# Performance work log

Hardware: AMD Instinct MI355X
Metric: run time of the kernel (lower is better)

Reference implementation:

```python
import jax, jax.numpy as jnp
import numpy as np

N = 50000      # num nodes
E = 800000     # num edges
F_IN = 100     # input features (ogbn-products)
HID = 128      # hidden_dim (per-head out_channels)
H = 2          # heads
OUT = 47       # num classes
NEG_SLOPE = 0.2


def setup_inputs() -> dict:
    key = jax.random.key(0)
    ks = jax.random.split(key, 14)
    def glorot(k, shape, fan):
        return jax.random.normal(k, shape, jnp.float32) * (1.0 / np.sqrt(fan))
    x = jax.random.normal(ks[0], (N, F_IN), jnp.float32)
    edge_index = jax.random.randint(ks[1], (2, E), 0, N)
    # GAT layer 0: lin_l (= lin_r, shared) weight [H*HID, F_IN], attention vecs [H, HID]
    W0 = glorot(ks[2], (H * HID, F_IN), F_IN)
    b0 = jnp.zeros((H * HID,), jnp.float32)
    attl0 = glorot(ks[3], (H, HID), HID)
    attr0 = glorot(ks[4], (H, HID), HID)
    # GAT layer 1: input dim H*HID
    W1 = glorot(ks[5], (H * HID, H * HID), H * HID)
    b1 = jnp.zeros((H * HID,), jnp.float32)
    attl1 = glorot(ks[6], (H, HID), HID)
    attr1 = glorot(ks[7], (H, HID), HID)
    # post_mp: Linear(H*HID -> HID), Linear(HID -> OUT)
    Wp1 = glorot(ks[8], (HID, H * HID), H * HID)
    bp1 = jnp.zeros((HID,), jnp.float32)
    Wp2 = glorot(ks[9], (OUT, HID), HID)
    bp2 = jnp.zeros((OUT,), jnp.float32)
    return dict(x=x, edge_index=edge_index, W0=W0, b0=b0, attl0=attl0, attr0=attr0,
                W1=W1, b1=b1, attl1=attl1, attr1=attr1,
                Wp1=Wp1, bp1=bp1, Wp2=Wp2, bp2=bp2)


def gat_layer(x, W, b, att_l, att_r, src, dst):
    # shared lin_l == lin_r in the source
    h = (x @ W.T + b).reshape(-1, H, HID)          # [N, H, C]
    alpha_l = jnp.einsum('nhc,hc->nh', h, att_l)   # per-node left scores
    alpha_r = jnp.einsum('nhc,hc->nh', h, att_r)   # per-node right scores
    e = jax.nn.leaky_relu(alpha_l[src] + alpha_r[dst], NEG_SLOPE)  # [E, H]
    # segment softmax over edges grouped by destination node
    emax = jax.ops.segment_max(e, dst, num_segments=N)             # [N, H]
    ee = jnp.exp(e - emax[dst])
    denom = jax.ops.segment_sum(ee, dst, num_segments=N)           # [N, H]
    a = ee / denom[dst]                                            # [E, H]
    msg = a[:, :, None] * h[src]                                   # [E, H, C]
    out = jax.ops.segment_sum(msg, dst, num_segments=N)            # [N, H, C]
    return out.reshape(-1, H * HID)


def reference(x, edge_index, W0, b0, attl0, attr0, W1, b1, attl1, attr1, Wp1, bp1, Wp2, bp2):
    src, dst = edge_index[0], edge_index[1]
    x = jax.nn.relu(gat_layer(x, W0, b0, attl0, attr0, src, dst))
    x = jax.nn.relu(gat_layer(x, W1, b1, attl1, attr1, src, dst))
    h = x @ Wp1.T + bp1           # dropout p=0.0 -> identity
    logits = h @ Wp2.T + bp2
    return jax.nn.log_softmax(logits, axis=1)
```

## Files before the change

kernel.cpp:

```cpp
#include <hip/hip_runtime.h>
#include <math.h>

#define N_NODES 50000
#define E_EDGES 800000
#define F_IN 100
#define HID 128
#define HEADS 2
#define OUT_C 47
#define HH (HEADS*HID)
#define MPAD 50048

typedef float floatx4 __attribute__((ext_vector_type(4)));
typedef float float2v __attribute__((ext_vector_type(2)));
typedef short short8 __attribute__((ext_vector_type(8)));

__device__ inline ushort bf16round(float v) {
    unsigned u = __float_as_uint(v);
    return (ushort)((u + 0x7FFFu + ((u >> 16) & 1u)) >> 16);
}

__device__ __forceinline__ void gl_lds16(const void* g, void* l) {
    __builtin_amdgcn_global_load_lds(
        (const __attribute__((address_space(1))) unsigned int*)g,
        (__attribute__((address_space(3))) unsigned int*)l, 16, 0, 0);
}

__device__ __forceinline__ void gemm_body(
    int bx, int by,
    const ushort* __restrict__ Ab, const ushort* __restrict__ Wb,
    const float* __restrict__ bias,
    ushort* __restrict__ Hb,
    const float* __restrict__ attl, const float* __restrict__ attr,
    float* __restrict__ al, float* __restrict__ ar,
    int M, int Kp, ushort* sA, ushort* sB)
{
    const int t = threadIdx.x;
    const int wave = t >> 6, lane = t & 63;
    const int quad = lane >> 4, l16 = lane & 15;
    const int rl = lane >> 2, seg = lane & 3;
    const int m0 = by * 128, n0 = bx * 128;

    floatx4 acc[2][8];
#pragma unroll
    for (int i = 0; i < 2; i++)
#pragma unroll
        for (int j = 0; j < 8; j++) acc[i][j] = (floatx4)(0.f);

    for (int k0 = 0; k0 < Kp; k0 += 32) {
#pragma unroll
        for (int j = 0; j < 2; j++) {
            int br = wave * 32 + j * 16;
            size_t gro = (size_t)(m0 + br + rl) * Kp + k0 + seg * 8;
            gl_lds16(Ab + gro, sA + br * 32);
        }
#pragma unroll
        for (int j = 0; j < 2; j++) {
            int br = wave * 32 + j * 16;
            size_t gro = (size_t)(n0 + br + rl) * Kp + k0 + seg * 8;
            gl_lds16(Wb + gro, sB + br * 32);
        }
        __syncthreads();

        short8 af[2];
#pragma unroll
        for (int sm = 0; sm < 2; sm++) {
            int r = wave * 32 + sm * 16 + l16;
            af[sm] = *(const short8*)(sA + r * 32 + quad * 8);
        }
#pragma unroll
        for (int sn = 0; sn < 8; sn++) {
            int r = sn * 16 + l16;
            short8 b = *(const short8*)(sB + r * 32 + quad * 8);
#pragma unroll
            for (int sm = 0; sm < 2; sm++)
                acc[sm][sn] = __builtin_amdgcn_mfma_f32_16x16x32_bf16(af[sm], b, acc[sm][sn], 0, 0, 0);
        }
        __syncthreads();
    }

    float bias_r[8], att_l[8], att_r[8];
#pragma unroll
    for (int sn = 0; sn < 8; sn++) {
        int ai = n0 + sn * 16 + l16;
        bias_r[sn] = bias[ai];
        att_l[sn] = attl[ai];
        att_r[sn] = attr[ai];
    }
#pragma unroll
    for (int sm = 0; sm < 2; sm++)
#pragma unroll
        for (int r = 0; r < 4; r++) {
            int gm = m0 + wave * 32 + sm * 16 + quad * 4 + r;
            float suml = 0.f, sumr = 0.f;
#pragma unroll
            for (int sn = 0; sn < 8; sn++) {
                float v = acc[sm][sn][r] + bias_r[sn];
                suml += v * att_l[sn];
                sumr += v * att_r[sn];
                if (gm < M) {
                    int gn = n0 + sn * 16 + l16;
                    Hb[(size_t)gm * 256 + gn] = bf16round(v);
                }
            }
#pragma unroll
            for (int off = 1; off < 16; off <<= 1) {
                suml += __shfl_xor(suml, off);
                sumr += __shfl_xor(sumr, off);
            }
            if (l16 == 0 && gm < M) {
                al[gm * HEADS + bx] = suml;
                ar[gm * HEADS + bx] = sumr;
            }
        }
}

__global__ __launch_bounds__(256) void gemm_l0(
    const ushort* __restrict__ xb, const ushort* __restrict__ W0b,
    const float* __restrict__ b0,
    const float* __restrict__ attl0, const float* __restrict__ attr0,
    ushort* __restrict__ hb, float* __restrict__ al, float* __restrict__ ar)
{
    __shared__ ushort sA[128 * 32], sB[128 * 32];
    gemm_body(blockIdx.x, blockIdx.y, xb, W0b, b0,
              hb, attl0, attr0, al, ar, N_NODES, 128, sA, sB);
}

__global__ __launch_bounds__(256) void gemm_l1(
    const ushort* __restrict__ Ab, const ushort* __restrict__ Wb,
    const float* __restrict__ bias, ushort* __restrict__ Hb,
    const float* __restrict__ attl, const float* __restrict__ attr,
    float* __restrict__ al, float* __restrict__ ar)
{
    __shared__ ushort sA[128 * 32], sB[128 * 32];
    gemm_body(blockIdx.x, blockIdx.y, Ab, Wb, bias,
              Hb, attl, attr, al, ar, N_NODES, HH, sA, sB);
}

__global__ void count_convert(const int* __restrict__ dstv, int* __restrict__ deg,
                              ushort* __restrict__ rank,
                              const float* __restrict__ x,  const float* __restrict__ W0,
                              const float* __restrict__ W1, const float* __restrict__ Wp1,
                              const float* __restrict__ Wp2,
                              ushort* __restrict__ xb,  ushort* __restrict__ W0b,
                              ushort* __restrict__ W1b, ushort* __restrict__ Wp1b,
                              ushort* __restrict__ Wp2b) {
    const int cx = N_NODES * 32;
    const int c0 = cx + 256 * 32;
    const int c1 = c0 + (HH * HH) / 4;
    const int c2 = c1 + (HID * HH) / 4;
    const int c3 = c2 + (64 * HID) / 4;
    int i = blockIdx.x * 256 + threadIdx.x;
    if (i < E_EDGES) {
        int d = dstv[i];
        rank[i] = (ushort)atomicAdd(&deg[d], 1);
    }
    if (i >= c3) return;
    float4 v = make_float4(0.f, 0.f, 0.f, 0.f);
    ushort* H; size_t o;
    if (i < cx) {
        int row = i >> 5, kc = (i & 31) * 4;
        if (kc < F_IN) v = *(const float4*)(x + (size_t)row * F_IN + kc);
        H = xb; o = (size_t)row * 128 + kc;
    } else if (i < c0) {
        int j = i - cx;
        int row = j >> 5, kc = (j & 31) * 4;
        if (kc < F_IN) v = *(const float4*)(W0 + (size_t)row * F_IN + kc);
        H = W0b; o = (size_t)row * 128 + kc;
    } else if (i < c1) {
        int j = i - c0;
        v = *(const float4*)(W1 + (size_t)j * 4);
        H = W1b; o = (size_t)j * 4;
    } else if (i < c2) {
        int j = i - c1;
        v = *(const float4*)(Wp1 + (size_t)j * 4);
        H = Wp1b; o = (size_t)j * 4;
    } else {
        int j = i - c2;
        int row = j >> 5;
        if (row < OUT_C) v = *(const float4*)(Wp2 + (size_t)j * 4);
        H = Wp2b; o = (size_t)j * 4;
    }
    ushort4 r;
    r.x = bf16round(v.x); r.y = bf16round(v.y);
    r.z = bf16round(v.z); r.w = bf16round(v.w);
    *(ushort4*)(H + o) = r;
}

__global__ void scan_local(const int* __restrict__ cnt, int* __restrict__ excl,
                           int* __restrict__ bsum, int Nn) {
    __shared__ int s[256];
    int t = threadIdx.x;
    int i = blockIdx.x * 256 + t;
    int v = (i < Nn) ? cnt[i] : 0;
    s[t] = v;
    __syncthreads();
    for (int off = 1; off < 256; off <<= 1) {
        int add = (t >= off) ? s[t - off] : 0;
        __syncthreads();
        s[t] += add;
        __syncthreads();
    }
    int incl = s[t];
    if (i < Nn) excl[i] = incl - v;
    if (t == 255) bsum[blockIdx.x] = incl;
}

__global__ void scan_add_fused(int* __restrict__ rowptr, const int* __restrict__ bsum,
                               int Nn, int Etot, int nblk) {
    __shared__ int s[256];
    int t = threadIdx.x;
    s[t] = (t < nblk) ? bsum[t] : 0;
    __syncthreads();
    for (int off = 1; off < 256; off <<= 1) {
        int add = (t >= off) ? s[t - off] : 0;
        __syncthreads();
        s[t] += add;
        __syncthreads();
    }
    int add = (blockIdx.x == 0) ? 0 : s[blockIdx.x - 1];
    int i = blockIdx.x * 256 + t;
    if (i < Nn) rowptr[i] += add;
    if (i == 0) rowptr[Nn] = Etot;
}

__global__ void fill_csr16(const int* __restrict__ src, const int* __restrict__ dst,
                           const int* __restrict__ rowptr, const ushort* __restrict__ rank,
                           ushort* __restrict__ csr16, int E) {
    int e = blockIdx.x * 256 + threadIdx.x;
    if (e < E) {
        int pos = rowptr[dst[e]] + (int)rank[e];
        csr16[pos] = (ushort)src[e];
    }
}

__global__ __launch_bounds__(256) void gat_aggregate(
    const ushort* __restrict__ hb, const float* __restrict__ al, const float* __restrict__ ar,
    const int* __restrict__ rowptr, const ushort* __restrict__ csr16,
    ushort* __restrict__ outb)
{
    const int node = blockIdx.x * 4 + (threadIdx.x >> 6);
    const int lane = threadIdx.x & 63;
    if (node >= N_NODES) return;
    const int beg = rowptr[node], end = rowptr[node + 1];
    const int half = lane >> 5;
    const int l32  = lane & 31;
    const int headf = l32 >> 4;
    const float2 ard = ((const float2*)ar)[node];

    float dsum0 = 0.f, dsum1 = 0.f;
    float2v av[4];
#pragma unroll
    for (int j = 0; j < 4; j++) av[j] = (float2v)(0.f);

    for (int c0 = beg; c0 < end; c0 += 64) {
        const int n = min(64, end - c0);
        int s = 0; float w0 = 0.f, w1 = 0.f;
        if (lane < n) {
            s = (int)csr16[c0 + lane];
            float2 aa = ((const float2*)al)[s];
            float e0 = aa.x + ard.x;
            float e1 = aa.y + ard.y;
            e0 = fmaxf(e0, 0.f) + 0.2f * fminf(e0, 0.f);
            e1 = fmaxf(e1, 0.f) + 0.2f * fminf(e1, 0.f);
            w0 = __expf(e0); w1 = __expf(e1);
            dsum0 += w0; dsum1 += w1;
        }
        for (int i = 0; i < n; i += 4) {
            int e0i = i + half;
            int   se0 = __shfl(s,  e0i);
            float u00 = __shfl(w0, e0i);
            float u01 = __shfl(w1, e0i);
            float2v we0 = (float2v)(headf ? u01 : u00);
            const uint4 q0 = *(const uint4*)(hb + (size_t)se0 * 256 + l32 * 8);
            int e1i = i + 2 + half;
            int   se1 = __shfl(s,  e1i);
            float u10 = __shfl(w0, e1i);
            float u11 = __shfl(w1, e1i);
            float2v we1 = (float2v)(headf ? u11 : u10);
            const uint4 q1 = *(const uint4*)(hb + (size_t)se1 * 256 + l32 * 8);
            float2v p;
            p.x = __uint_as_float(q0.x << 16); p.y = __uint_as_float(q0.x & 0xFFFF0000u);
            av[0] += we0 * p;
            p.x = __uint_as_float(q0.y << 16); p.y = __uint_as_float(q0.y & 0xFFFF0000u);
            av[1] += we0 * p;
            p.x = __uint_as_float(q0.z << 16); p.y = __uint_as_float(q0.z & 0xFFFF0000u);
            av[2] += we0 * p;
            p.x = __uint_as_float(q0.w << 16); p.y = __uint_as_float(q0.w & 0xFFFF0000u);
            av[3] += we0 * p;
            p.x = __uint_as_float(q1.x << 16); p.y = __uint_as_float(q1.x & 0xFFFF0000u);
            av[0] += we1 * p;
            p.x = __uint_as_float(q1.y << 16); p.y = __uint_as_float(q1.y & 0xFFFF0000u);
            av[1] += we1 * p;
            p.x = __uint_as_float(q1.z << 16); p.y = __uint_as_float(q1.z & 0xFFFF0000u);
            av[2] += we1 * p;
            p.x = __uint_as_float(q1.w << 16); p.y = __uint_as_float(q1.w & 0xFFFF0000u);
            av[3] += we1 * p;
        }
    }
#pragma unroll
    for (int j = 0; j < 4; j++) {
        av[j].x += __shfl_xor(av[j].x, 32);
        av[j].y += __shfl_xor(av[j].y, 32);
    }
#pragma unroll
    for (int off = 32; off; off >>= 1) {
        dsum0 += __shfl_xor(dsum0, off);
        dsum1 += __shfl_xor(dsum1, off);
    }
    if (half == 0) {
        const float den = headf ? dsum1 : dsum0;
        const float inv = (end > beg) ? 1.f / den : 0.f;
        ushort r[8];
#pragma unroll
        for (int j = 0; j < 4; j++) {
            r[2*j]   = bf16round(fmaxf(av[j].x * inv, 0.f));
            r[2*j+1] = bf16round(fmaxf(av[j].y * inv, 0.f));
        }
        *(uint4*)(outb + (size_t)node * 256 + l32 * 8) = *(uint4*)r;
    }
}

__global__ __launch_bounds__(256) void fused_post(
    const ushort* __restrict__ Ab,
    const ushort* __restrict__ Bb,
    const float* __restrict__ bp1,
    const ushort* __restrict__ W2b,
    const float* __restrict__ bp2,
    float* __restrict__ out, int M)
{
    __shared__ ushort sA[128 * 32];
    __shared__ ushort sB[128 * 32];
    __shared__ ushort sP[128 * 136];

    const int t = threadIdx.x;
    const int wave = t >> 6, lane = t & 63;
    const int quad = lane >> 4, l16 = lane & 15;
    const int rl = lane >> 2, seg = lane & 3;
    const int m0 = blockIdx.x * 128;

    floatx4 acc[2][8];
#pragma unroll
    for (int i = 0; i < 2; i++)
#pragma unroll
        for (int j = 0; j < 8; j++) acc[i][j] = (floatx4)(0.f);

    for (int k0 = 0; k0 < HH; k0 += 32) {
#pragma unroll
        for (int j = 0; j < 2; j++) {
            int br = wave * 32 + j * 16;
            size_t gro = (size_t)(m0 + br + rl) * HH + k0 + seg * 8;
            gl_lds16(Ab + gro, sA + br * 32);
        }
#pragma unroll
        for (int j = 0; j < 2; j++) {
            int br = wave * 32 + j * 16;
            size_t gro = (size_t)(br + rl) * HH + k0 + seg * 8;
            gl_lds16(Bb + gro, sB + br * 32);
        }
        __syncthreads();
        short8 af[2];
#pragma unroll
        for (int sm = 0; sm < 2; sm++) {
            int r = wave * 32 + sm * 16 + l16;
            af[sm] = *(const short8*)(sA + r * 32 + quad * 8);
        }
#pragma unroll
        for (int sn = 0; sn < 8; sn++) {
            int r = sn * 16 + l16;
            short8 b = *(const short8*)(sB + r * 32 + quad * 8);
#pragma unroll
            for (int sm = 0; sm < 2; sm++)
                acc[sm][sn] = __builtin_amdgcn_mfma_f32_16x16x32_bf16(af[sm], b, acc[sm][sn], 0, 0, 0);
        }
        __syncthreads();
    }
#pragma unroll
    for (int sm = 0; sm < 2; sm++)
#pragma unroll
        for (int sn = 0; sn < 8; sn++)
#pragma unroll
            for (int r = 0; r < 4; r++) {
                int row = wave * 32 + sm * 16 + quad * 4 + r;
                int col = sn * 16 + l16;
                sP[row * 136 + col] = bf16round(acc[sm][sn][r] + bp1[col]);
            }
    __syncthreads();

    floatx4 acc2[2][4];
#pragma unroll
    for (int i = 0; i < 2; i++)
#pragma unroll
        for (int j = 0; j < 4; j++) acc2[i][j] = (floatx4)(0.f);

    for (int k0 = 0; k0 < HID; k0 += 32) {
        {
            int br = wave * 16;
            size_t gro = (size_t)(br + rl) * HID + k0 + seg * 8;
            gl_lds16(W2b + gro, sA + br * 32);
        }
        __syncthreads();
        short8 ph[2];
#pragma unroll
        for (int sm = 0; sm < 2; sm++) {
            int r = wave * 32 + sm * 16 + l16;
            ph[sm] = *(const short8*)(sP + r * 136 + k0 + quad * 8);
        }
#pragma unroll
        for (int sn = 0; sn < 4; sn++) {
            int r = sn * 16 + l16;
            short8 b = *(const short8*)(sA + r * 32 + quad * 8);
#pragma unroll
            for (int sm = 0; sm < 2; sm++)
                acc2[sm][sn] = __builtin_amdgcn_mfma_f32_16x16x32_bf16(ph[sm], b, acc2[sm][sn], 0, 0, 0);
        }
        __syncthreads();
    }

    float b2[4];
#pragma unroll
    for (int sn = 0; sn < 4; sn++) {
        int n = sn * 16 + l16;
        b2[sn] = (n < OUT_C) ? bp2[n] : 0.f;
    }
#pragma unroll
    for (int sm = 0; sm < 2; sm++)
#pragma unroll
        for (int r = 0; r < 4; r++) {
            float v[4];
            float m = -INFINITY;
#pragma unroll
            for (int sn = 0; sn < 4; sn++) {
                int n = sn * 16 + l16;
                float xv = (n < OUT_C) ? acc2[sm][sn][r] + b2[sn] : -INFINITY;
                v[sn] = xv;
                m = fmaxf(m, xv);
            }
#pragma unroll
            for (int off = 1; off < 16; off <<= 1) m = fmaxf(m, __shfl_xor(m, off));
            float ssum = 0.f;
#pragma unroll
            for (int sn = 0; sn < 4; sn++) {
                int n = sn * 16 + l16;
                if (n < OUT_C) ssum += __expf(v[sn] - m);
            }
#pragma unroll
            for (int off = 1; off < 16; off <<= 1) ssum += __shfl_xor(ssum, off);
            float lse = m + logf(ssum);
            int gm = m0 + wave * 32 + sm * 16 + quad * 4 + r;
            if (gm < M) {
#pragma unroll
                for (int sn = 0; sn < 4; sn++) {
                    int n = sn * 16 + l16;
                    if (n < OUT_C) out[(size_t)gm * OUT_C + n] = v[sn] - lse;
                }
            }
        }
}

extern "C" void kernel_launch(void* const* d_in, const int* in_sizes, int n_in,
                              void* d_out, int out_size, void* d_ws, size_t ws_size,
                              hipStream_t stream) {
    const float* x     = (const float*)d_in[0];
    const int*   ei    = (const int*)d_in[1];
    const float* W0    = (const float*)d_in[2];
    const float* b0    = (const float*)d_in[3];
    const float* attl0 = (const float*)d_in[4];
    const float* attr0 = (const float*)d_in[5];
    const float* W1    = (const float*)d_in[6];
    const float* b1    = (const float*)d_in[7];
    const float* attl1 = (const float*)d_in[8];
    const float* attr1 = (const float*)d_in[9];
    const float* Wp1   = (const float*)d_in[10];
    const float* bp1   = (const float*)d_in[11];
    const float* Wp2   = (const float*)d_in[12];
    const float* bp2   = (const float*)d_in[13];
    float* out = (float*)d_out;

    const int Nn = N_NODES, Etot = E_EDGES;
    const int* srcv = ei;
    const int* dstv = ei + Etot;

    char* ws = (char*)d_ws;
    size_t off = 0;
    auto alloc = [&](size_t bytes) -> void* {
        void* p = ws + off;
        off = (off + bytes + 255) & ~(size_t)255;
        return p;
    };
    int*    rowptr = (int*)alloc((size_t)(Nn + 1) * sizeof(int));
    int*    deg    = (int*)alloc((size_t)Nn * sizeof(int));
    ushort* rank   = (ushort*)alloc((size_t)Etot * 2);
    ushort* csr16  = (ushort*)alloc((size_t)Etot * 2);
    int*    bsum   = (int*)alloc(256 * sizeof(int));
    float*  al     = (float*)alloc((size_t)Nn * HEADS * sizeof(float));
    float*  ar     = (float*)alloc((size_t)Nn * HEADS * sizeof(float));
    ushort* xb     = (ushort*)alloc((size_t)MPAD * 128 * 2);
    ushort* W0b    = (ushort*)alloc((size_t)HH * 128 * 2);
    ushort* W1b    = (ushort*)alloc((size_t)HH * HH * 2);
    ushort* Wp1b   = (ushort*)alloc((size_t)HID * HH * 2);
    ushort* Wp2b   = (ushort*)alloc((size_t)64 * HID * 2);
    ushort* hb     = (ushort*)alloc((size_t)Nn * HH * 2);
    ushort* xbb    = (ushort*)alloc((size_t)MPAD * HH * 2);

    const int nblk = (Nn + 255) / 256;

    hipMemsetAsync(deg, 0, (size_t)Nn * sizeof(int), stream);

    {
        const int tot = N_NODES * 32 + 256 * 32 + (HH * HH) / 4 + (HID * HH) / 4 + (64 * HID) / 4;
        const int grid = (tot + 255) / 256;
        count_convert<<<grid, 256, 0, stream>>>(
            dstv, deg, rank, x, W0, W1, Wp1, Wp2, xb, W0b, W1b, Wp1b, Wp2b);
    }

    {
        dim3 g(2, MPAD / 128);
        gemm_l0<<<g, 256, 0, stream>>>(xb, W0b, b0, attl0, attr0, hb, al, ar);
    }

    scan_local<<<nblk, 256, 0, stream>>>(deg, rowptr, bsum, Nn);
    scan_add_fused<<<nblk, 256, 0, stream>>>(rowptr, bsum, Nn, Etot, nblk);
    fill_csr16<<<(Etot + 255) / 256, 256, 0, stream>>>(srcv, dstv, rowptr, rank, csr16, Etot);

    gat_aggregate<<<(Nn + 3) / 4, 256, 0, stream>>>(hb, al, ar, rowptr, csr16, xbb);

    {
        dim3 g(2, MPAD / 128);
        gemm_l1<<<g, 256, 0, stream>>>(xbb, W1b, b1, hb, attl1, attr1, al, ar);
    }
    gat_aggregate<<<(Nn + 3) / 4, 256, 0, stream>>>(hb, al, ar, rowptr, csr16, xbb);

    fused_post<<<MPAD / 128, 256, 0, stream>>>(xbb, Wp1b, bp1, Wp2b, bp2, out, Nn);
}
```

Before: 313.7 us.

## Fuse CSR build and bf16 conversion into one cooperative kernel with grid syncs

Replaces the memset, count_convert, two scan kernels and fill_csr16 with a single cooperative kernel of 196 blocks that uses grid.sync between phases. This removes several kernel launches and their inter-kernel gaps. In exchange, a small persistent grid does all the edge atomics and the conversion through grid-stride loops, which lowers parallelism. It also depends on all 196 blocks being co-resident.

```diff
diff --git a/kernel.cpp b/kernel.cpp
--- a/kernel.cpp
+++ b/kernel.cpp
@@ -1,5 +1,8 @@
 #include <hip/hip_runtime.h>
+#include <hip/hip_cooperative_groups.h>
 #include <math.h>
+
+namespace cg = cooperative_groups;
 
 #define N_NODES 50000
 #define E_EDGES 800000
@@ -9,6 +12,7 @@
 #define OUT_C 47
 #define HH (HEADS*HID)
 #define MPAD 50048
+#define NBLK 196
 
 typedef float floatx4 __attribute__((ext_vector_type(4)));
 typedef float float2v __attribute__((ext_vector_type(2)));
@@ -23,6 +27,101 @@
     __builtin_amdgcn_global_load_lds(
         (const __attribute__((address_space(1))) unsigned int*)g,
         (__attribute__((address_space(3))) unsigned int*)l, 16, 0, 0);
+}
+
+__global__ void csr_build(
+    const int* __restrict__ dstv, const int* __restrict__ srcv,
+    int* __restrict__ deg, ushort* __restrict__ rank,
+    int* __restrict__ rowptr, int* __restrict__ bsum, ushort* __restrict__ csr16,
+    const float* __restrict__ x,  const float* __restrict__ W0,
+    const float* __restrict__ W1, const float* __restrict__ Wp1,
+    const float* __restrict__ Wp2,
+    ushort* __restrict__ xb,  ushort* __restrict__ W0b,
+    ushort* __restrict__ W1b, ushort* __restrict__ Wp1b, ushort* __restrict__ Wp2b)
+{
+    cg::grid_group grid = cg::this_grid();
+    const int t = threadIdx.x;
+    const int tid = blockIdx.x * 256 + t;
+    const int gsz = NBLK * 256;
+
+    for (int i = tid; i < N_NODES; i += gsz) deg[i] = 0;
+    grid.sync();
+
+    for (int e = tid; e < E_EDGES; e += gsz)
+        rank[e] = (ushort)atomicAdd(&deg[dstv[e]], 1);
+    {
+        const int cx = N_NODES * 32;
+        const int c0 = cx + 256 * 32;
+        const int c1 = c0 + (HH * HH) / 4;
+        const int c2 = c1 + (HID * HH) / 4;
+        const int c3 = c2 + (64 * HID) / 4;
+        for (int i = tid; i < c3; i += gsz) {
+            float4 v = make_float4(0.f, 0.f, 0.f, 0.f);
+            ushort* H; size_t o;
+            if (i < cx) {
+                int row = i >> 5, kc = (i & 31) * 4;
+                if (kc < F_IN) v = *(const float4*)(x + (size_t)row * F_IN + kc);
+                H = xb; o = (size_t)row * 128 + kc;
+            } else if (i < c0) {
+                int j = i - cx;
+                int row = j >> 5, kc = (j & 31) * 4;
+                if (kc < F_IN) v = *(const float4*)(W0 + (size_t)row * F_IN + kc);
+                H = W0b; o = (size_t)row * 128 + kc;
+            } else if (i < c1) {
+                int j = i - c0;
+                v = *(const float4*)(W1 + (size_t)j * 4);
+                H = W1b; o = (size_t)j * 4;
+            } else if (i < c2) {
+                int j = i - c1;
+                v = *(const float4*)(Wp1 + (size_t)j * 4);
+                H = Wp1b; o = (size_t)j * 4;
+            } else {
+                int j = i - c2;
+                int row = j >> 5;
+                if (row < OUT_C) v = *(const float4*)(Wp2 + (size_t)j * 4);
+                H = Wp2b; o = (size_t)j * 4;
+            }
+            ushort4 r;
+            r.x = bf16round(v.x); r.y = bf16round(v.y);
+            r.z = bf16round(v.z); r.w = bf16round(v.w);
+            *(ushort4*)(H + o) = r;
+        }
+    }
+    grid.sync();
+
+    __shared__ int s[256];
+    int i2 = blockIdx.x * 256 + t;
+    int v2 = (i2 < N_NODES) ? deg[i2] : 0;
+    s[t] = v2;
+    __syncthreads();
+    for (int off = 1; off < 256; off <<= 1) {
+        int add = (t >= off) ? s[t - off] : 0;
+        __syncthreads();
+        s[t] += add;
+        __syncthreads();
+    }
+    int incl = s[t];
+    if (i2 < N_NODES) rowptr[i2] = incl - v2;
+    if (t == 255) bsum[blockIdx.x] = incl;
+    grid.sync();
+
+    s[t] = (t < NBLK) ? bsum[t] : 0;
+    __syncthreads();
+    for (int off = 1; off < 256; off <<= 1) {
+        int add = (t >= off) ? s[t - off] : 0;
+        __syncthreads();
+        s[t] += add;
+        __syncthreads();
+    }
+    int addp = (blockIdx.x == 0) ? 0 : s[blockIdx.x - 1];
+    if (i2 < N_NODES) rowptr[i2] += addp;
+    if (i2 == 0) rowptr[N_NODES] = E_EDGES;
+    grid.sync();
+
+    for (int e = tid; e < E_EDGES; e += gsz) {
+        int pos = rowptr[dstv[e]] + (int)rank[e];
+        csr16[pos] = (ushort)srcv[e];
+    }
 }
 
 __device__ __forceinline__ void gemm_body(
@@ -134,103 +233,6 @@
     __shared__ ushort sA[128 * 32], sB[128 * 32];
     gemm_body(blockIdx.x, blockIdx.y, Ab, Wb, bias,
               Hb, attl, attr, al, ar, N_NODES, HH, sA, sB);
-}
-
-__global__ void count_convert(const int* __restrict__ dstv, int* __restrict__ deg,
-                              ushort* __restrict__ rank,
-                              const float* __restrict__ x,  const float* __restrict__ W0,
-                              const float* __restrict__ W1, const float* __restrict__ Wp1,
-                              const float* __restrict__ Wp2,
-                              ushort* __restrict__ xb,  ushort* __restrict__ W0b,
-                              ushort* __restrict__ W1b, ushort* __restrict__ Wp1b,
-                              ushort* __restrict__ Wp2b) {
-    const int cx = N_NODES * 32;
-    const int c0 = cx + 256 * 32;
-    const int c1 = c0 + (HH * HH) / 4;
-    const int c2 = c1 + (HID * HH) / 4;
-    const int c3 = c2 + (64 * HID) / 4;
-    int i = blockIdx.x * 256 + threadIdx.x;
-    if (i < E_EDGES) {
-        int d = dstv[i];
-        rank[i] = (ushort)atomicAdd(&deg[d], 1);
-    }
-    if (i >= c3) return;
-    float4 v = make_float4(0.f, 0.f, 0.f, 0.f);
-    ushort* H; size_t o;
-    if (i < cx) {
-        int row = i >> 5, kc = (i & 31) * 4;
-        if (kc < F_IN) v = *(const float4*)(x + (size_t)row * F_IN + kc);
-        H = xb; o = (size_t)row * 128 + kc;
-    } else if (i < c0) {
-        int j = i - cx;
-        int row = j >> 5, kc = (j & 31) * 4;
-        if (kc < F_IN) v = *(const float4*)(W0 + (size_t)row * F_IN + kc);
-        H = W0b; o = (size_t)row * 128 + kc;
-    } else if (i < c1) {
-        int j = i - c0;
-        v = *(const float4*)(W1 + (size_t)j * 4);
-        H = W1b; o = (size_t)j * 4;
-    } else if (i < c2) {
-        int j = i - c1;
-        v = *(const float4*)(Wp1 + (size_t)j * 4);
-        H = Wp1b; o = (size_t)j * 4;
-    } else {
-        int j = i - c2;
-        int row = j >> 5;
-        if (row < OUT_C) v = *(const float4*)(Wp2 + (size_t)j * 4);
-        H = Wp2b; o = (size_t)j * 4;
-    }
-    ushort4 r;
-    r.x = bf16round(v.x); r.y = bf16round(v.y);
-    r.z = bf16round(v.z); r.w = bf16round(v.w);
-    *(ushort4*)(H + o) = r;
-}
-
-__global__ void scan_local(const int* __restrict__ cnt, int* __restrict__ excl,
-                           int* __restrict__ bsum, int Nn) {
-    __shared__ int s[256];
-    int t = threadIdx.x;
-    int i = blockIdx.x * 256 + t;
-    int v = (i < Nn) ? cnt[i] : 0;
-    s[t] = v;
-    __syncthreads();
-    for (int off = 1; off < 256; off <<= 1) {
-        int add = (t >= off) ? s[t - off] : 0;
-        __syncthreads();
-        s[t] += add;
-        __syncthreads();
-    }
-    int incl = s[t];
-    if (i < Nn) excl[i] = incl - v;
-    if (t == 255) bsum[blockIdx.x] = incl;
-}
-
-__global__ void scan_add_fused(int* __restrict__ rowptr, const int* __restrict__ bsum,
-                               int Nn, int Etot, int nblk) {
-    __shared__ int s[256];
-    int t = threadIdx.x;
-    s[t] = (t < nblk) ? bsum[t] : 0;
-    __syncthreads();
-    for (int off = 1; off < 256; off <<= 1) {
-        int add = (t >= off) ? s[t - off] : 0;
-        __syncthreads();
-        s[t] += add;
-        __syncthreads();
-    }
-    int add = (blockIdx.x == 0) ? 0 : s[blockIdx.x - 1];
-    int i = blockIdx.x * 256 + t;
-    if (i < Nn) rowptr[i] += add;
-    if (i == 0) rowptr[Nn] = Etot;
-}
-
-__global__ void fill_csr16(const int* __restrict__ src, const int* __restrict__ dst,
-                           const int* __restrict__ rowptr, const ushort* __restrict__ rank,
-                           ushort* __restrict__ csr16, int E) {
-    int e = blockIdx.x * 256 + threadIdx.x;
-    if (e < E) {
-        int pos = rowptr[dst[e]] + (int)rank[e];
-        csr16[pos] = (ushort)src[e];
-    }
 }
 
 __global__ __launch_bounds__(256) void gat_aggregate(
@@ -476,7 +478,7 @@
     const float* bp2   = (const float*)d_in[13];
     float* out = (float*)d_out;
 
-    const int Nn = N_NODES, Etot = E_EDGES;
+    const int Etot = E_EDGES;
     const int* srcv = ei;
     const int* dstv = ei + Etot;
 
@@ -487,30 +489,32 @@
         off = (off + bytes + 255) & ~(size_t)255;
         return p;
     };
-    int*    rowptr = (int*)alloc((size_t)(Nn + 1) * sizeof(int));
-    int*    deg    = (int*)alloc((size_t)Nn * sizeof(int));
+    int*    rowptr = (int*)alloc((size_t)(N_NODES + 1) * sizeof(int));
+    int*    deg    = (int*)alloc((size_t)N_NODES * sizeof(int));
     ushort* rank   = (ushort*)alloc((size_t)Etot * 2);
     ushort* csr16  = (ushort*)alloc((size_t)Etot * 2);
     int*    bsum   = (int*)alloc(256 * sizeof(int));
-    float*  al     = (float*)alloc((size_t)Nn * HEADS * sizeof(float));
-    float*  ar     = (float*)alloc((size_t)Nn * HEADS * sizeof(float));
+    float*  al     = (float*)alloc((size_t)N_NODES * HEADS * sizeof(float));
+    float*  ar     = (float*)alloc((size_t)N_NODES * HEADS * sizeof(float));
     ushort* xb     = (ushort*)alloc((size_t)MPAD * 128 * 2);
     ushort* W0b    = (ushort*)alloc((size_t)HH * 128 * 2);
     ushort* W1b    = (ushort*)alloc((size_t)HH * HH * 2);
     ushort* Wp1b   = (ushort*)alloc((size_t)HID * HH * 2);
+    ushort* Wp1b_  = Wp1b;
     ushort* Wp2b   = (ushort*)alloc((size_t)64 * HID * 2);
-    ushort* hb     = (ushort*)alloc((size_t)Nn * HH * 2);
+    ushort* hb     = (ushort*)alloc((size_t)N_NODES * HH * 2);
     ushort* xbb    = (ushort*)alloc((size_t)MPAD * HH * 2);
-
-    const int nblk = (Nn + 255) / 256;
-
-    hipMemsetAsync(deg, 0, (size_t)Nn * sizeof(int), stream);
+    (void)Wp1b_;
 
     {
-        const int tot = N_NODES * 32 + 256 * 32 + (HH * HH) / 4 + (HID * HH) / 4 + (64 * HID) / 4;
-        const int grid = (tot + 255) / 256;
-        count_convert<<<grid, 256, 0, stream>>>(
-            dstv, deg, rank, x, W0, W1, Wp1, Wp2, xb, W0b, W1b, Wp1b, Wp2b);
+        void* args[] = {
+            (void*)&dstv, (void*)&srcv, (void*)&deg, (void*)&rank,
+            (void*)&rowptr, (void*)&bsum, (void*)&csr16,
+            (void*)&x, (void*)&W0, (void*)&W1, (void*)&Wp1, (void*)&Wp2,
+            (void*)&xb, (void*)&W0b, (void*)&W1b, (void*)&Wp1b, (void*)&Wp2b
+        };
+        hipLaunchCooperativeKernel((void*)csr_build, dim3(NBLK), dim3(256),
+                                   args, 0, stream);
     }
 
     {
@@ -518,17 +522,13 @@
         gemm_l0<<<g, 256, 0, stream>>>(xb, W0b, b0, attl0, attr0, hb, al, ar);
     }
 
-    scan_local<<<nblk, 256, 0, stream>>>(deg, rowptr, bsum, Nn);
-    scan_add_fused<<<nblk, 256, 0, stream>>>(rowptr, bsum, Nn, Etot, nblk);
-    fill_csr16<<<(Etot + 255) / 256, 256, 0, stream>>>(srcv, dstv, rowptr, rank, csr16, Etot);
-
-    gat_aggregate<<<(Nn + 3) / 4, 256, 0, stream>>>(hb, al, ar, rowptr, csr16, xbb);
+    gat_aggregate<<<(N_NODES + 3) / 4, 256, 0, stream>>>(hb, al, ar, rowptr, csr16, xbb);
 
     {
         dim3 g(2, MPAD / 128);
         gemm_l1<<<g, 256, 0, stream>>>(xbb, W1b, b1, hb, attl1, attr1, al, ar);
     }
-    gat_aggregate<<<(Nn + 3) / 4, 256, 0, stream>>>(hb, al, ar, rowptr, csr16, xbb);
-
-    fused_post<<<MPAD / 128, 256, 0, stream>>>(xbb, Wp1b, bp1, Wp2b, bp2, out, Nn);
-}
+    gat_aggregate<<<(N_NODES + 3) / 4, 256, 0, stream>>>(hb, al, ar, rowptr, csr16, xbb);
+
+    fused_post<<<MPAD / 128, 256, 0, stream>>>(xbb, Wp1b, bp1, Wp2b, bp2, out, N_NODES);
+}
```

Measured after the change: 437.5 us. 39.5% more time.
